# Performance work log

Measured on AMD Instinct MI355X. Metric: run time of the kernel, lower is better.

## Reference

```python
import jax, jax.numpy as jnp
import numpy as np

B, N, E, D_IN, D_OUT = 16, 2048, 65536, 256, 256


def setup_inputs() -> dict:
    key = jax.random.key(0)
    k1, k2, k3 = jax.random.split(key, 3)
    node_features = jax.random.normal(k1, (B, N, D_IN), dtype=jnp.float32)
    edge_indices = jax.random.randint(k2, (B, 2, E), 0, N, dtype=jnp.int64)
    W = jax.random.normal(k3, (D_OUT, 2 * D_IN), dtype=jnp.float32) * (1.0 / np.sqrt(2 * D_IN))
    b = jnp.zeros((D_OUT,), dtype=jnp.float32)
    return {"node_features": node_features, "edge_indices": edge_indices, "W": W, "b": b}


def reference(node_features, edge_indices, W, b):
    # node_features: [B, N, D]; edge_indices: [B, 2, E] (src row 0, dst row 1)
    n_nodes = node_features.shape[1]
    src = edge_indices[:, 0, :]  # [B, E]
    dst = edge_indices[:, 1, :]  # [B, E]
    # gather source-node features per edge: [B, E, D]
    gathered = jnp.take_along_axis(node_features, src[:, :, None], axis=1)

    def per_graph(feats_g, dst_g):
        s = jax.ops.segment_sum(feats_g, dst_g, num_segments=n_nodes)          # [N, D]
        c = jax.ops.segment_sum(jnp.ones_like(dst_g, dtype=feats_g.dtype),
                                dst_g, num_segments=n_nodes)                    # [N]
        return s / jnp.maximum(c, 1.0)[:, None]  # mean; 0 for isolated nodes

    neighbor_agg = jax.vmap(per_graph)(gathered, dst)            # [B, N, D]
    combined = jnp.concatenate([node_features, neighbor_agg], axis=-1)  # [B, N, 2D]
    return jnp.einsum('bnd,od->bno', combined, W) + b
```

## Files before the change

### kernel.cpp

```cpp
#include <hip/hip_runtime.h>
#include <hip/hip_bf16.h>

#define BATCH 16
#define NNODE 2048
#define NEDGE 65536
#define DIN   256
#define DOUT  256
#define KDIM  512
#define SUB   16
#define ESUB  (NEDGE/SUB)

typedef __attribute__((ext_vector_type(8))) short short8;
typedef __attribute__((ext_vector_type(8))) ushort ushort8;
typedef __attribute__((ext_vector_type(4))) float f32x4;

__device__ __forceinline__ ushort f2bf(float f) {
    union { float f; unsigned u; } v; v.f = f;
    unsigned u = v.u;
    unsigned r = (u + 0x7fffu + ((u >> 16) & 1u)) >> 16;
    return (ushort)r;
}

__device__ __forceinline__ int q8(float x) {
    float c = fminf(fmaxf(x * 16.0f, -127.0f), 127.0f);
    return (int)rintf(c);
}

#define ASYNC_COPY16(gsrc, ldst) \
    __builtin_amdgcn_global_load_lds((const __attribute__((address_space(1))) void*)(gsrc), \
                                     (__attribute__((address_space(3))) void*)(ldst), 16, 0, 0)

__global__ __launch_bounds__(256) void prep_kernel(
        const float* __restrict__ X, const float* __restrict__ W,
        const int* __restrict__ E,
        int* __restrict__ partial,
        ushort* __restrict__ Xbf, unsigned char* __restrict__ Xi8,
        ushort* __restrict__ Wbf) {
    int bid = blockIdx.x;
    int t = threadIdx.x;
    if (bid < 256) {
        __shared__ int hist[NNODE];
        int b = bid & 15, sub = bid >> 4;
#pragma unroll
        for (int j = 0; j < 8; ++j) hist[t + j * 256] = 0;
        __syncthreads();
        const int4* dsts = reinterpret_cast<const int4*>(
            E + (size_t)b * 2 * NEDGE + NEDGE + sub * ESUB);
#pragma unroll
        for (int j = 0; j < 4; ++j) {
            int4 d = dsts[j * 256 + t];
            atomicAdd(&hist[d.x], 1);
            atomicAdd(&hist[d.y], 1);
            atomicAdd(&hist[d.z], 1);
            atomicAdd(&hist[d.w], 1);
        }
        __syncthreads();
        int* pb = partial + ((size_t)b * SUB + sub) * NNODE;
#pragma unroll
        for (int j = 0; j < 8; ++j) pb[t + j * 256] = hist[t + j * 256];
    } else if (bid < 4352) {
        size_t i = (size_t)(bid - 256) * 256 + t;
        const float4* p = reinterpret_cast<const float4*>(X + i * 8);
        float4 u = p[0], v = p[1];
        ushort4 o0 = { f2bf(u.x), f2bf(u.y), f2bf(u.z), f2bf(u.w) };
        ushort4 o1 = { f2bf(v.x), f2bf(v.y), f2bf(v.z), f2bf(v.w) };
        *reinterpret_cast<ushort4*>(Xbf + i * 8)     = o0;
        *reinterpret_cast<ushort4*>(Xbf + i * 8 + 4) = o1;
        unsigned q0 = (q8(u.x) & 255) | ((q8(u.y) & 255) << 8) |
                      ((q8(u.z) & 255) << 16) | ((unsigned)(q8(u.w) & 255) << 24);
        unsigned q1 = (q8(v.x) & 255) | ((q8(v.y) & 255) << 8) |
                      ((q8(v.z) & 255) << 16) | ((unsigned)(q8(v.w) & 255) << 24);
        uint2 q = { q0, q1 };
        *reinterpret_cast<uint2*>(Xi8 + i * 8) = q;
    } else {
        size_t i = (size_t)(bid - 4352) * 256 + t;
        const float4* p = reinterpret_cast<const float4*>(W + i * 8);
        float4 u = p[0], v = p[1];
        ushort4 o0 = { f2bf(u.x), f2bf(u.y), f2bf(u.z), f2bf(u.w) };
        ushort4 o1 = { f2bf(v.x), f2bf(v.y), f2bf(v.z), f2bf(v.w) };
        *reinterpret_cast<ushort4*>(Wbf + i * 8)     = o0;
        *reinterpret_cast<ushort4*>(Wbf + i * 8 + 4) = o1;
    }
}

__global__ __launch_bounds__(256) void fillscan_kernel(
        const int* __restrict__ E,
        const int* __restrict__ partial,
        int* __restrict__ counts, int* __restrict__ cursor,
        int* __restrict__ srcIdx) {
    __shared__ int cur[NNODE];
    __shared__ int tsum[256];
    int bid = blockIdx.x;
    int t = threadIdx.x;
    int b = bid & 15, sub = bid >> 4;
    const int* pb = partial + (size_t)b * SUB * NNODE;

    int tot[8] = {}, pre[8] = {};
    for (int k = 0; k < SUB; ++k) {
        const int4* p = reinterpret_cast<const int4*>(pb + k * NNODE + t * 8);
        int4 a = p[0], c = p[1];
        if (k < sub) {
            pre[0] += a.x; pre[1] += a.y; pre[2] += a.z; pre[3] += a.w;
            pre[4] += c.x; pre[5] += c.y; pre[6] += c.z; pre[7] += c.w;
        }
        tot[0] += a.x; tot[1] += a.y; tot[2] += a.z; tot[3] += a.w;
        tot[4] += c.x; tot[5] += c.y; tot[6] += c.z; tot[7] += c.w;
    }
    int s = 0;
#pragma unroll
    for (int j = 0; j < 8; ++j) s += tot[j];
    tsum[t] = s;
    __syncthreads();
    for (int off = 1; off < 256; off <<= 1) {
        int v = (t >= off) ? tsum[t - off] : 0;
        __syncthreads();
        tsum[t] += v;
        __syncthreads();
    }
    int run = (t == 0) ? 0 : tsum[t - 1];
    bool writer = (sub == 0);
    int base = b * NNODE + t * 8;
#pragma unroll
    for (int j = 0; j < 8; ++j) {
        cur[t * 8 + j] = run + pre[j];
        if (writer) { counts[base + j] = tot[j]; cursor[base + j] = run; }
        run += tot[j];
    }
    __syncthreads();

    const int* eb = E + (size_t)b * 2 * NEDGE;
    const int4* srcs = reinterpret_cast<const int4*>(eb + sub * ESUB);
    const int4* dsts = reinterpret_cast<const int4*>(eb + NEDGE + sub * ESUB);
    int* sb = srcIdx + (size_t)b * NEDGE;
#pragma unroll
    for (int j = 0; j < 4; ++j) {
        int4 sv = srcs[j * 256 + t];
        int4 dv = dsts[j * 256 + t];
        sb[atomicAdd(&cur[dv.x], 1)] = sv.x;
        sb[atomicAdd(&cur[dv.y], 1)] = sv.y;
        sb[atomicAdd(&cur[dv.z], 1)] = sv.z;
        sb[atomicAdd(&cur[dv.w], 1)] = sv.w;
    }
}

__global__ __launch_bounds__(256) void aggregate_kernel(
        const unsigned char* __restrict__ Xi8,
        const int* __restrict__ srcIdx,
        const int* __restrict__ cursor,
        const int* __restrict__ counts,
        ushort* __restrict__ Gbf) {
    int bid = blockIdx.x;
    int blk = (bid & 7) * 1024 + (bid >> 3);
    int wave = threadIdx.x >> 6;
    int lane = threadIdx.x & 63;
    int q = lane >> 4;
    int l16 = lane & 15;
    int f0 = l16 * 16;
    int node = blk * 4 + wave;
    int b = node >> 11;
    int deg = counts[node];
    int start = cursor[node];
    const unsigned char* xb = Xi8 + (size_t)b * NNODE * DIN;
    const int* sidx = srcIdx + (size_t)b * NEDGE + start;

    unsigned a0 = 0, a1 = 0, a2 = 0, a3 = 0, a4 = 0, a5 = 0, a6 = 0, a7 = 0;
#define M16 0x00FF00FFu
#define ACC16(v) do {                                                         \
        unsigned w0 = (v).x ^ 0x80808080u, w1 = (v).y ^ 0x80808080u;          \
        unsigned w2 = (v).z ^ 0x80808080u, w3 = (v).w ^ 0x80808080u;          \
        a0 += w0 & M16;  a1 += (w0 >> 8) & M16;                               \
        a2 += w1 & M16;  a3 += (w1 >> 8) & M16;                               \
        a4 += w2 & M16;  a5 += (w2 >> 8) & M16;                               \
        a6 += w3 & M16;  a7 += (w3 >> 8) & M16;                               \
    } while (0)

    int i = 0;
    for (; i + 16 <= deg; i += 16) {
        int s0 = sidx[i + q], s1 = sidx[i + 4 + q];
        int s2 = sidx[i + 8 + q], s3 = sidx[i + 12 + q];
        uint4 v0 = *reinterpret_cast<const uint4*>(xb + (size_t)s0 * DIN + f0);
        uint4 v1 = *reinterpret_cast<const uint4*>(xb + (size_t)s1 * DIN + f0);
        uint4 v2 = *reinterpret_cast<const uint4*>(xb + (size_t)s2 * DIN + f0);
        uint4 v3 = *reinterpret_cast<const uint4*>(xb + (size_t)s3 * DIN + f0);
        ACC16(v0); ACC16(v1); ACC16(v2); ACC16(v3);
    }
    for (; i < deg; i += 4) {
        int e = i + q;
        uint4 v = { 0x80808080u, 0x80808080u, 0x80808080u, 0x80808080u };
        if (e < deg) {
            int s0 = sidx[e];
            v = *reinterpret_cast<const uint4*>(xb + (size_t)s0 * DIN + f0);
        }
        ACC16(v);
    }
#undef ACC16
    a0 += (unsigned)__shfl_xor((int)a0, 16, 64); a0 += (unsigned)__shfl_xor((int)a0, 32, 64);
    a1 += (unsigned)__shfl_xor((int)a1, 16, 64); a1 += (unsigned)__shfl_xor((int)a1, 32, 64);
    a2 += (unsigned)__shfl_xor((int)a2, 16, 64); a2 += (unsigned)__shfl_xor((int)a2, 32, 64);
    a3 += (unsigned)__shfl_xor((int)a3, 16, 64); a3 += (unsigned)__shfl_xor((int)a3, 32, 64);
    a4 += (unsigned)__shfl_xor((int)a4, 16, 64); a4 += (unsigned)__shfl_xor((int)a4, 32, 64);
    a5 += (unsigned)__shfl_xor((int)a5, 16, 64); a5 += (unsigned)__shfl_xor((int)a5, 32, 64);
    a6 += (unsigned)__shfl_xor((int)a6, 16, 64); a6 += (unsigned)__shfl_xor((int)a6, 32, 64);
    a7 += (unsigned)__shfl_xor((int)a7, 16, 64); a7 += (unsigned)__shfl_xor((int)a7, 32, 64);

    if (q == 0) {
        float sc = 1.0f / (16.0f * (float)max(deg, 1));
        float bias = 128.0f * (float)deg;
        float f[16];
        f[ 0] = ((float)(int)(a0 & 0xFFFFu) - bias) * sc;
        f[ 2] = ((float)(int)(a0 >> 16)     - bias) * sc;
        f[ 1] = ((float)(int)(a1 & 0xFFFFu) - bias) * sc;
        f[ 3] = ((float)(int)(a1 >> 16)     - bias) * sc;
        f[ 4] = ((float)(int)(a2 & 0xFFFFu) - bias) * sc;
        f[ 6] = ((float)(int)(a2 >> 16)     - bias) * sc;
        f[ 5] = ((float)(int)(a3 & 0xFFFFu) - bias) * sc;
        f[ 7] = ((float)(int)(a3 >> 16)     - bias) * sc;
        f[ 8] = ((float)(int)(a4 & 0xFFFFu) - bias) * sc;
        f[10] = ((float)(int)(a4 >> 16)     - bias) * sc;
        f[ 9] = ((float)(int)(a5 & 0xFFFFu) - bias) * sc;
        f[11] = ((float)(int)(a5 >> 16)     - bias) * sc;
        f[12] = ((float)(int)(a6 & 0xFFFFu) - bias) * sc;
        f[14] = ((float)(int)(a6 >> 16)     - bias) * sc;
        f[13] = ((float)(int)(a7 & 0xFFFFu) - bias) * sc;
        f[15] = ((float)(int)(a7 >> 16)     - bias) * sc;
        ushort8 o0, o1;
#pragma unroll
        for (int j = 0; j < 8; ++j) { o0[j] = f2bf(f[j]); o1[j] = f2bf(f[j + 8]); }
        ushort* gp = Gbf + (size_t)node * DIN + f0;
        *reinterpret_cast<ushort8*>(gp)     = o0;
        *reinterpret_cast<ushort8*>(gp + 8) = o1;
    }
}

__global__ __launch_bounds__(256) void gemm_kernel(
        const ushort* __restrict__ Xbf,
        const ushort* __restrict__ Gbf,
        const ushort* __restrict__ Wbf,
        const float* __restrict__ bias,
        float* __restrict__ out) {
    __shared__ ushort As[3][128 * 32];
    __shared__ ushort Bs[3][128 * 32];
    const int tid = threadIdx.x;
    const int wid = tid >> 6, lane = tid & 63;

    int orig = blockIdx.x;
    int logical = (orig & 7) * 64 + (orig >> 3);
    int bx = logical >> 1;
    int by = logical & 1;
    const int rowBase = bx * 128;
    const int colBase = by * 128;
    const int wm = wid >> 1, wn = wid & 1;

    f32x4 acc[4][4] = {};

    const int lr = lane >> 2;
    const int lk = (((lane & 3) ^ ((lane >> 3) & 3)) * 8);

    const ushort* Arow = Xbf + (size_t)rowBase * DIN;
    const ushort* Grow = Gbf + (size_t)rowBase * DIN;
    const ushort* Brow = Wbf + (size_t)colBase * KDIM;
    const int r0 = wid * 16 + lr;

#define STAGE(k0, buf) do {                                                   \
        const ushort* Ab = ((k0) < DIN) ? (Arow + (k0)) : (Grow + ((k0) - DIN)); \
        const ushort* Bb = Brow + (k0);                                       \
        ASYNC_COPY16(Ab + (size_t)r0 * DIN + lk,          &As[buf][wid * 512]);       \
        ASYNC_COPY16(Ab + (size_t)(r0 + 64) * DIN + lk,   &As[buf][2048 + wid * 512]);\
        ASYNC_COPY16(Bb + (size_t)r0 * KDIM + lk,         &Bs[buf][wid * 512]);       \
        ASYNC_COPY16(Bb + (size_t)(r0 + 64) * KDIM + lk,  &Bs[buf][2048 + wid * 512]);\
    } while (0)

    const int fl = lane & 15;
    const int fc = ((lane >> 4) ^ ((fl >> 1) & 3)) * 8;

    STAGE(0, 0);
    STAGE(32, 1);
    for (int t = 0; t < 16; ++t) {
        const int bt = t % 3;
        if (t + 2 < 16) {
            STAGE((t + 2) * 32, (t + 2) % 3);
            asm volatile("s_waitcnt vmcnt(8)" ::: "memory");
        } else if (t + 1 < 16) {
            asm volatile("s_waitcnt vmcnt(4)" ::: "memory");
        } else {
            asm volatile("s_waitcnt vmcnt(0)" ::: "memory");
        }
        __builtin_amdgcn_s_barrier();

        short8 a[4], b[4];
#pragma unroll
        for (int m = 0; m < 4; ++m)
            a[m] = *reinterpret_cast<const short8*>(
                &As[bt][(wm * 64 + m * 16 + fl) * 32 + fc]);
#pragma unroll
        for (int n = 0; n < 4; ++n)
            b[n] = *reinterpret_cast<const short8*>(
                &Bs[bt][(wn * 64 + n * 16 + fl) * 32 + fc]);
#pragma unroll
        for (int m = 0; m < 4; ++m)
#pragma unroll
            for (int n = 0; n < 4; ++n)
                acc[m][n] = __builtin_amdgcn_mfma_f32_16x16x32_bf16(
                    a[m], b[n], acc[m][n], 0, 0, 0);
        __builtin_amdgcn_s_barrier();
    }
#undef STAGE

    const int cl = lane & 15, rq = lane >> 4;
#pragma unroll
    for (int n = 0; n < 4; ++n) {
        int col = colBase + wn * 64 + n * 16 + cl;
        float bv = bias[col];
#pragma unroll
        for (int m = 0; m < 4; ++m) {
            int r0o = rowBase + wm * 64 + m * 16 + rq * 4;
#pragma unroll
            for (int j = 0; j < 4; ++j)
                out[(size_t)(r0o + j) * DOUT + col] = acc[m][n][j] + bv;
        }
    }
}

extern "C" void kernel_launch(void* const* d_in, const int* in_sizes, int n_in,
                              void* d_out, int out_size, void* d_ws, size_t ws_size,
                              hipStream_t stream) {
    const float* X    = (const float*)d_in[0];
    const int*   E    = (const int*)d_in[1];
    const float* W    = (const float*)d_in[2];
    const float* bias = (const float*)d_in[3];
    float* out = (float*)d_out;

    char* ws = (char*)d_ws;
    ushort* Xbf  = (ushort*)ws;
    ushort* Gbf  = Xbf + (size_t)BATCH * NNODE * DIN;
    ushort* Wbf  = Gbf + (size_t)BATCH * NNODE * DIN;
    int* counts  = (int*)(Wbf + (size_t)DOUT * KDIM);
    int* cursor  = counts + BATCH * NNODE;
    int* srcIdx  = cursor + BATCH * NNODE;
    unsigned char* Xi8 = (unsigned char*)(srcIdx + (size_t)BATCH * NEDGE);
    int* partial = (int*)Gbf;

    prep_kernel<<<4416, 256, 0, stream>>>(X, W, E, partial, Xbf, Xi8, Wbf);

    fillscan_kernel<<<256, 256, 0, stream>>>(E, partial, counts, cursor, srcIdx);

    aggregate_kernel<<<(BATCH * NNODE) / 4, 256, 0, stream>>>(
        Xi8, srcIdx, cursor, counts, Gbf);

    dim3 ggrid(512);
    gemm_kernel<<<ggrid, 256, 0, stream>>>(Xbf, Gbf, Wbf, bias, out);
}
```

Before: 66.91 us.

## Fuse neighbor aggregation into GEMM with FP8 aggregated half in LDS

Removes the separate aggregate kernel and the bf16 G buffer round trip through global memory. Each 512-thread GEMM block now computes the mean-aggregated neighbor features for its 128 rows, quantizes them to FP8 e4m3 in LDS, and runs the second half of K with fp8 MFMA against an FP8 pre-swizzled copy of W. Blocks cover all 256 output columns, so each gathers its rows once. In exchange the gather latency is no longer overlapped with other blocks' GEMM, there are only 256 blocks, and FP8 costs accuracy.

```diff
diff --git a/kernel.cpp b/kernel.cpp
--- a/kernel.cpp
+++ b/kernel.cpp
@@ -11,7 +11,6 @@
 #define ESUB  (NEDGE/SUB)
 
 typedef __attribute__((ext_vector_type(8))) short short8;
-typedef __attribute__((ext_vector_type(8))) ushort ushort8;
 typedef __attribute__((ext_vector_type(4))) float f32x4;
 
 __device__ __forceinline__ ushort f2bf(float f) {
@@ -26,6 +25,36 @@
     return (int)rintf(c);
 }
 
+__device__ __forceinline__ unsigned f2e4m3(float x) {
+    unsigned u = __float_as_uint(x);
+    unsigned s = (u >> 24) & 0x80u;
+    float ax = __uint_as_float(u & 0x7FFFFFFFu);
+    if (ax >= 448.0f) return s | 0x7Eu;
+    if (ax < 0.0009765625f) return s;
+    if (ax < 0.015625f) {
+        int q = (int)rintf(ax * 512.0f);
+        return s | (unsigned)q;
+    }
+    unsigned au = __float_as_uint(ax);
+    int e = (int)((au >> 23) & 0xFF) - 127;
+    unsigned m = au & 0x7FFFFFu;
+    unsigned keep = m >> 20;
+    unsigned rest = m & 0xFFFFFu;
+    keep += (rest > 0x80000u) || (rest == 0x80000u && (keep & 1u));
+    unsigned val = ((unsigned)(e + 7) << 3) + keep;
+    if (val > 0x7Eu) val = 0x7Eu;
+    return s | val;
+}
+template <bool HI>
+__device__ __forceinline__ unsigned pk2_fp8(float a, float b, unsigned old) {
+#if __has_builtin(__builtin_amdgcn_cvt_pk_fp8_f32)
+    return (unsigned)__builtin_amdgcn_cvt_pk_fp8_f32(a, b, (int)old, HI);
+#else
+    unsigned p = f2e4m3(a) | (f2e4m3(b) << 8);
+    return HI ? ((old & 0xFFFFu) | (p << 16)) : ((old & 0xFFFF0000u) | p);
+#endif
+}
+
 #define ASYNC_COPY16(gsrc, ldst) \
     __builtin_amdgcn_global_load_lds((const __attribute__((address_space(1))) void*)(gsrc), \
                                      (__attribute__((address_space(3))) void*)(ldst), 16, 0, 0)
@@ -35,7 +64,7 @@
         const int* __restrict__ E,
         int* __restrict__ partial,
         ushort* __restrict__ Xbf, unsigned char* __restrict__ Xi8,
-        ushort* __restrict__ Wbf) {
+        ushort* __restrict__ Wbf, unsigned char* __restrict__ Wf8s) {
     int bid = blockIdx.x;
     int t = threadIdx.x;
     if (bid < 256) {
@@ -73,13 +102,26 @@
         uint2 q = { q0, q1 };
         *reinterpret_cast<uint2*>(Xi8 + i * 8) = q;
     } else {
-        size_t i = (size_t)(bid - 4352) * 256 + t;
-        const float4* p = reinterpret_cast<const float4*>(W + i * 8);
+        int i = (bid - 4352) * 256 + t;
+        int col = i >> 6;
+        int k = (i & 63) * 8;
+        const float4* p = reinterpret_cast<const float4*>(W + (size_t)col * KDIM + k);
         float4 u = p[0], v = p[1];
-        ushort4 o0 = { f2bf(u.x), f2bf(u.y), f2bf(u.z), f2bf(u.w) };
-        ushort4 o1 = { f2bf(v.x), f2bf(v.y), f2bf(v.z), f2bf(v.w) };
-        *reinterpret_cast<ushort4*>(Wbf + i * 8)     = o0;
-        *reinterpret_cast<ushort4*>(Wbf + i * 8 + 4) = o1;
+        if (k < DIN) {
+            ushort4 o0 = { f2bf(u.x), f2bf(u.y), f2bf(u.z), f2bf(u.w) };
+            ushort4 o1 = { f2bf(v.x), f2bf(v.y), f2bf(v.z), f2bf(v.w) };
+            *reinterpret_cast<ushort4*>(Wbf + (size_t)col * KDIM + k)     = o0;
+            *reinterpret_cast<ushort4*>(Wbf + (size_t)col * KDIM + k + 4) = o1;
+        } else {
+            unsigned w0 = pk2_fp8<false>(u.x, u.y, 0u);
+            w0 = pk2_fp8<true>(u.z, u.w, w0);
+            unsigned w1 = pk2_fp8<false>(v.x, v.y, 0u);
+            w1 = pk2_fp8<true>(v.z, v.w, w1);
+            int kk = k - DIN;
+            int kt = kk >> 5, kq = (kk >> 3) & 3;
+            uint2 qv = { w0, w1 };
+            *reinterpret_cast<uint2*>(Wf8s + (size_t)kt * 8192 + kq * 2048 + col * 8) = qv;
+        }
     }
 }
 
@@ -143,27 +185,50 @@
     }
 }
 
-__global__ __launch_bounds__(256) void aggregate_kernel(
+__global__ __launch_bounds__(512, 4) void gemm_fused(
+        const ushort* __restrict__ Xbf,
         const unsigned char* __restrict__ Xi8,
+        const ushort* __restrict__ Wbf,
+        const unsigned char* __restrict__ Wf8s,
         const int* __restrict__ srcIdx,
         const int* __restrict__ cursor,
         const int* __restrict__ counts,
-        ushort* __restrict__ Gbf) {
-    int bid = blockIdx.x;
-    int blk = (bid & 7) * 1024 + (bid >> 3);
-    int wave = threadIdx.x >> 6;
-    int lane = threadIdx.x & 63;
-    int q = lane >> 4;
-    int l16 = lane & 15;
-    int f0 = l16 * 16;
-    int node = blk * 4 + wave;
-    int b = node >> 11;
-    int deg = counts[node];
-    int start = cursor[node];
-    const unsigned char* xb = Xi8 + (size_t)b * NNODE * DIN;
-    const int* sidx = srcIdx + (size_t)b * NEDGE + start;
-
-    unsigned a0 = 0, a1 = 0, a2 = 0, a3 = 0, a4 = 0, a5 = 0, a6 = 0, a7 = 0;
+        const float* __restrict__ bias,
+        float* __restrict__ out) {
+    __shared__ ushort As[2][128 * 32];
+    __shared__ ushort Bs[2][256 * 32];
+    __shared__ uint4  GqV[2048];
+
+    const int tid = threadIdx.x;
+    const int wid = tid >> 6, lane = tid & 63;
+    const int wm = wid >> 2, wn = wid & 3;
+
+    int orig = blockIdx.x;
+    int logical = (orig & 7) * 32 + (orig >> 3);
+    const int rowBase = logical * 128;
+    const int b = rowBase >> 11;
+
+    f32x4 acc[4][4] = {};
+
+    const int r0 = wid * 16 + (lane >> 2);
+    const int lk = (((lane & 3) ^ ((lane >> 3) & 3)) * 8);
+    const ushort* Arow = Xbf + (size_t)rowBase * DIN;
+
+#define STAGE_X(k0, buf) do {                                                  \
+        ASYNC_COPY16(Arow + (size_t)r0 * DIN + (k0) + lk,         &As[buf][wid * 512]);        \
+        ASYNC_COPY16(Wbf + (size_t)r0 * KDIM + (k0) + lk,         &Bs[buf][wid * 512]);        \
+        ASYNC_COPY16(Wbf + (size_t)(r0 + 128) * KDIM + (k0) + lk, &Bs[buf][4096 + wid * 512]); \
+    } while (0)
+#define STAGE_G(kt, fbuf) \
+        ASYNC_COPY16(Wf8s + (size_t)(kt) * 8192 + (size_t)(wid * 64 + lane) * 16, \
+                     &Bs[fbuf][wid * 512])
+
+    STAGE_X(0, 0);
+
+    {
+        const int q = lane >> 4, l16 = lane & 15;
+        const int f0 = l16 * 16;
+        const unsigned char* xb = Xi8 + (size_t)b * NNODE * DIN;
 #define M16 0x00FF00FFu
 #define ACC16(v) do {                                                         \
         unsigned w0 = (v).x ^ 0x80808080u, w1 = (v).y ^ 0x80808080u;          \
@@ -173,143 +238,141 @@
         a4 += w2 & M16;  a5 += (w2 >> 8) & M16;                               \
         a6 += w3 & M16;  a7 += (w3 >> 8) & M16;                               \
     } while (0)
-
-    int i = 0;
-    for (; i + 16 <= deg; i += 16) {
-        int s0 = sidx[i + q], s1 = sidx[i + 4 + q];
-        int s2 = sidx[i + 8 + q], s3 = sidx[i + 12 + q];
-        uint4 v0 = *reinterpret_cast<const uint4*>(xb + (size_t)s0 * DIN + f0);
-        uint4 v1 = *reinterpret_cast<const uint4*>(xb + (size_t)s1 * DIN + f0);
-        uint4 v2 = *reinterpret_cast<const uint4*>(xb + (size_t)s2 * DIN + f0);
-        uint4 v3 = *reinterpret_cast<const uint4*>(xb + (size_t)s3 * DIN + f0);
-        ACC16(v0); ACC16(v1); ACC16(v2); ACC16(v3);
-    }
-    for (; i < deg; i += 4) {
-        int e = i + q;
-        uint4 v = { 0x80808080u, 0x80808080u, 0x80808080u, 0x80808080u };
-        if (e < deg) {
-            int s0 = sidx[e];
-            v = *reinterpret_cast<const uint4*>(xb + (size_t)s0 * DIN + f0);
-        }
-        ACC16(v);
-    }
+        for (int nn = 0; nn < 16; ++nn) {
+            int r = wid * 16 + nn;
+            int node = rowBase + r;
+            int deg = counts[node];
+            int start = cursor[node];
+            const int* sidx = srcIdx + (size_t)b * NEDGE + start;
+            unsigned a0 = 0, a1 = 0, a2 = 0, a3 = 0, a4 = 0, a5 = 0, a6 = 0, a7 = 0;
+            int i = 0;
+            for (; i + 16 <= deg; i += 16) {
+                int s0 = sidx[i + q], s1 = sidx[i + 4 + q];
+                int s2 = sidx[i + 8 + q], s3 = sidx[i + 12 + q];
+                uint4 v0 = *reinterpret_cast<const uint4*>(xb + (size_t)s0 * DIN + f0);
+                uint4 v1 = *reinterpret_cast<const uint4*>(xb + (size_t)s1 * DIN + f0);
+                uint4 v2 = *reinterpret_cast<const uint4*>(xb + (size_t)s2 * DIN + f0);
+                uint4 v3 = *reinterpret_cast<const uint4*>(xb + (size_t)s3 * DIN + f0);
+                ACC16(v0); ACC16(v1); ACC16(v2); ACC16(v3);
+            }
+            for (; i < deg; i += 4) {
+                int e = i + q;
+                uint4 v = { 0x80808080u, 0x80808080u, 0x80808080u, 0x80808080u };
+                if (e < deg)
+                    v = *reinterpret_cast<const uint4*>(xb + (size_t)sidx[e] * DIN + f0);
+                ACC16(v);
+            }
+            a0 += (unsigned)__shfl_xor((int)a0, 16, 64); a0 += (unsigned)__shfl_xor((int)a0, 32, 64);
+            a1 += (unsigned)__shfl_xor((int)a1, 16, 64); a1 += (unsigned)__shfl_xor((int)a1, 32, 64);
+            a2 += (unsigned)__shfl_xor((int)a2, 16, 64); a2 += (unsigned)__shfl_xor((int)a2, 32, 64);
+            a3 += (unsigned)__shfl_xor((int)a3, 16, 64); a3 += (unsigned)__shfl_xor((int)a3, 32, 64);
+            a4 += (unsigned)__shfl_xor((int)a4, 16, 64); a4 += (unsigned)__shfl_xor((int)a4, 32, 64);
+            a5 += (unsigned)__shfl_xor((int)a5, 16, 64); a5 += (unsigned)__shfl_xor((int)a5, 32, 64);
+            a6 += (unsigned)__shfl_xor((int)a6, 16, 64); a6 += (unsigned)__shfl_xor((int)a6, 32, 64);
+            a7 += (unsigned)__shfl_xor((int)a7, 16, 64); a7 += (unsigned)__shfl_xor((int)a7, 32, 64);
+            if (q == 0) {
+                float sc = 1.0f / (16.0f * (float)max(deg, 1));
+                float bs = 128.0f * (float)deg;
+                float f[16];
+                f[ 0] = ((float)(int)(a0 & 0xFFFFu) - bs) * sc;
+                f[ 2] = ((float)(int)(a0 >> 16)     - bs) * sc;
+                f[ 1] = ((float)(int)(a1 & 0xFFFFu) - bs) * sc;
+                f[ 3] = ((float)(int)(a1 >> 16)     - bs) * sc;
+                f[ 4] = ((float)(int)(a2 & 0xFFFFu) - bs) * sc;
+                f[ 6] = ((float)(int)(a2 >> 16)     - bs) * sc;
+                f[ 5] = ((float)(int)(a3 & 0xFFFFu) - bs) * sc;
+                f[ 7] = ((float)(int)(a3 >> 16)     - bs) * sc;
+                f[ 8] = ((float)(int)(a4 & 0xFFFFu) - bs) * sc;
+                f[10] = ((float)(int)(a4 >> 16)     - bs) * sc;
+                f[ 9] = ((float)(int)(a5 & 0xFFFFu) - bs) * sc;
+                f[11] = ((float)(int)(a5 >> 16)     - bs) * sc;
+                f[12] = ((float)(int)(a6 & 0xFFFFu) - bs) * sc;
+                f[14] = ((float)(int)(a6 >> 16)     - bs) * sc;
+                f[13] = ((float)(int)(a7 & 0xFFFFu) - bs) * sc;
+                f[15] = ((float)(int)(a7 >> 16)     - bs) * sc;
+                unsigned wds[4];
+#pragma unroll
+                for (int w = 0; w < 4; ++w) {
+                    unsigned t0 = pk2_fp8<false>(f[4 * w], f[4 * w + 1], 0u);
+                    wds[w] = pk2_fp8<true>(f[4 * w + 2], f[4 * w + 3], t0);
+                }
+                int slot = l16 ^ ((r >> 1) & 7);
+                uint4 val;
+                if (r & 1) { val.x = wds[2]; val.y = wds[3]; val.z = wds[0]; val.w = wds[1]; }
+                else       { val.x = wds[0]; val.y = wds[1]; val.z = wds[2]; val.w = wds[3]; }
+                GqV[r * 16 + slot] = val;
+            }
+        }
 #undef ACC16
-    a0 += (unsigned)__shfl_xor((int)a0, 16, 64); a0 += (unsigned)__shfl_xor((int)a0, 32, 64);
-    a1 += (unsigned)__shfl_xor((int)a1, 16, 64); a1 += (unsigned)__shfl_xor((int)a1, 32, 64);
-    a2 += (unsigned)__shfl_xor((int)a2, 16, 64); a2 += (unsigned)__shfl_xor((int)a2, 32, 64);
-    a3 += (unsigned)__shfl_xor((int)a3, 16, 64); a3 += (unsigned)__shfl_xor((int)a3, 32, 64);
-    a4 += (unsigned)__shfl_xor((int)a4, 16, 64); a4 += (unsigned)__shfl_xor((int)a4, 32, 64);
-    a5 += (unsigned)__shfl_xor((int)a5, 16, 64); a5 += (unsigned)__shfl_xor((int)a5, 32, 64);
-    a6 += (unsigned)__shfl_xor((int)a6, 16, 64); a6 += (unsigned)__shfl_xor((int)a6, 32, 64);
-    a7 += (unsigned)__shfl_xor((int)a7, 16, 64); a7 += (unsigned)__shfl_xor((int)a7, 32, 64);
-
-    if (q == 0) {
-        float sc = 1.0f / (16.0f * (float)max(deg, 1));
-        float bias = 128.0f * (float)deg;
-        float f[16];
-        f[ 0] = ((float)(int)(a0 & 0xFFFFu) - bias) * sc;
-        f[ 2] = ((float)(int)(a0 >> 16)     - bias) * sc;
-        f[ 1] = ((float)(int)(a1 & 0xFFFFu) - bias) * sc;
-        f[ 3] = ((float)(int)(a1 >> 16)     - bias) * sc;
-        f[ 4] = ((float)(int)(a2 & 0xFFFFu) - bias) * sc;
-        f[ 6] = ((float)(int)(a2 >> 16)     - bias) * sc;
-        f[ 5] = ((float)(int)(a3 & 0xFFFFu) - bias) * sc;
-        f[ 7] = ((float)(int)(a3 >> 16)     - bias) * sc;
-        f[ 8] = ((float)(int)(a4 & 0xFFFFu) - bias) * sc;
-        f[10] = ((float)(int)(a4 >> 16)     - bias) * sc;
-        f[ 9] = ((float)(int)(a5 & 0xFFFFu) - bias) * sc;
-        f[11] = ((float)(int)(a5 >> 16)     - bias) * sc;
-        f[12] = ((float)(int)(a6 & 0xFFFFu) - bias) * sc;
-        f[14] = ((float)(int)(a6 >> 16)     - bias) * sc;
-        f[13] = ((float)(int)(a7 & 0xFFFFu) - bias) * sc;
-        f[15] = ((float)(int)(a7 >> 16)     - bias) * sc;
-        ushort8 o0, o1;
-#pragma unroll
-        for (int j = 0; j < 8; ++j) { o0[j] = f2bf(f[j]); o1[j] = f2bf(f[j + 8]); }
-        ushort* gp = Gbf + (size_t)node * DIN + f0;
-        *reinterpret_cast<ushort8*>(gp)     = o0;
-        *reinterpret_cast<ushort8*>(gp + 8) = o1;
-    }
-}
-
-__global__ __launch_bounds__(256) void gemm_kernel(
-        const ushort* __restrict__ Xbf,
-        const ushort* __restrict__ Gbf,
-        const ushort* __restrict__ Wbf,
-        const float* __restrict__ bias,
-        float* __restrict__ out) {
-    __shared__ ushort As[3][128 * 32];
-    __shared__ ushort Bs[3][128 * 32];
-    const int tid = threadIdx.x;
-    const int wid = tid >> 6, lane = tid & 63;
-
-    int orig = blockIdx.x;
-    int logical = (orig & 7) * 64 + (orig >> 3);
-    int bx = logical >> 1;
-    int by = logical & 1;
-    const int rowBase = bx * 128;
-    const int colBase = by * 128;
-    const int wm = wid >> 1, wn = wid & 1;
-
-    f32x4 acc[4][4] = {};
-
-    const int lr = lane >> 2;
-    const int lk = (((lane & 3) ^ ((lane >> 3) & 3)) * 8);
-
-    const ushort* Arow = Xbf + (size_t)rowBase * DIN;
-    const ushort* Grow = Gbf + (size_t)rowBase * DIN;
-    const ushort* Brow = Wbf + (size_t)colBase * KDIM;
-    const int r0 = wid * 16 + lr;
-
-#define STAGE(k0, buf) do {                                                   \
-        const ushort* Ab = ((k0) < DIN) ? (Arow + (k0)) : (Grow + ((k0) - DIN)); \
-        const ushort* Bb = Brow + (k0);                                       \
-        ASYNC_COPY16(Ab + (size_t)r0 * DIN + lk,          &As[buf][wid * 512]);       \
-        ASYNC_COPY16(Ab + (size_t)(r0 + 64) * DIN + lk,   &As[buf][2048 + wid * 512]);\
-        ASYNC_COPY16(Bb + (size_t)r0 * KDIM + lk,         &Bs[buf][wid * 512]);       \
-        ASYNC_COPY16(Bb + (size_t)(r0 + 64) * KDIM + lk,  &Bs[buf][2048 + wid * 512]);\
-    } while (0)
+#undef M16
+    }
+    __syncthreads();
 
     const int fl = lane & 15;
-    const int fc = ((lane >> 4) ^ ((fl >> 1) & 3)) * 8;
-
-    STAGE(0, 0);
-    STAGE(32, 1);
+    const int kq = lane >> 4;
+    const int fc = (kq ^ ((fl >> 1) & 3)) * 8;
+    const long* GqL = reinterpret_cast<const long*>(GqV);
+
     for (int t = 0; t < 16; ++t) {
-        const int bt = t % 3;
-        if (t + 2 < 16) {
-            STAGE((t + 2) * 32, (t + 2) % 3);
-            asm volatile("s_waitcnt vmcnt(8)" ::: "memory");
-        } else if (t + 1 < 16) {
-            asm volatile("s_waitcnt vmcnt(4)" ::: "memory");
+        if (t < 7) {
+            STAGE_X((t + 1) * 32, (t + 1) & 1);
+            asm volatile("s_waitcnt vmcnt(3)" ::: "memory");
+        } else if (t < 15) {
+            STAGE_G(t - 7, (t - 7) & 1);
+            asm volatile("s_waitcnt vmcnt(1)" ::: "memory");
         } else {
             asm volatile("s_waitcnt vmcnt(0)" ::: "memory");
         }
         __builtin_amdgcn_s_barrier();
 
-        short8 a[4], b[4];
-#pragma unroll
-        for (int m = 0; m < 4; ++m)
-            a[m] = *reinterpret_cast<const short8*>(
-                &As[bt][(wm * 64 + m * 16 + fl) * 32 + fc]);
-#pragma unroll
-        for (int n = 0; n < 4; ++n)
-            b[n] = *reinterpret_cast<const short8*>(
-                &Bs[bt][(wn * 64 + n * 16 + fl) * 32 + fc]);
-#pragma unroll
-        for (int m = 0; m < 4; ++m)
+        if (t < 8) {
+            const int bufx = t & 1;
+            short8 a[4], bb[4];
+#pragma unroll
+            for (int m = 0; m < 4; ++m)
+                a[m] = *reinterpret_cast<const short8*>(
+                    &As[bufx][(wm * 64 + m * 16 + fl) * 32 + fc]);
 #pragma unroll
             for (int n = 0; n < 4; ++n)
-                acc[m][n] = __builtin_amdgcn_mfma_f32_16x16x32_bf16(
-                    a[m], b[n], acc[m][n], 0, 0, 0);
+                bb[n] = *reinterpret_cast<const short8*>(
+                    &Bs[bufx][(wn * 64 + n * 16 + fl) * 32 + fc]);
+#pragma unroll
+            for (int m = 0; m < 4; ++m)
+#pragma unroll
+                for (int n = 0; n < 4; ++n)
+                    acc[m][n] = __builtin_amdgcn_mfma_f32_16x16x32_bf16(
+                        a[m], bb[n], acc[m][n], 0, 0, 0);
+        } else {
+            const int kt = t - 8;
+            const unsigned char* Bf8 =
+                reinterpret_cast<const unsigned char*>(&Bs[kt & 1][0]);
+            long ag[4], bg[4];
+#pragma unroll
+            for (int m = 0; m < 4; ++m) {
+                int r = wm * 64 + m * 16 + fl;
+                ag[m] = GqL[r * 32 + ((kt * 4 + kq) ^ (r & 15))];
+            }
+#pragma unroll
+            for (int n = 0; n < 4; ++n) {
+                int c = wn * 64 + n * 16 + fl;
+                bg[n] = *reinterpret_cast<const long*>(Bf8 + kq * 2048 + c * 8);
+            }
+#pragma unroll
+            for (int m = 0; m < 4; ++m)
+#pragma unroll
+                for (int n = 0; n < 4; ++n)
+                    acc[m][n] = __builtin_amdgcn_mfma_f32_16x16x32_fp8_fp8(
+                        ag[m], bg[n], acc[m][n], 0, 0, 0);
+        }
         __builtin_amdgcn_s_barrier();
     }
-#undef STAGE
+#undef STAGE_X
+#undef STAGE_G
 
     const int cl = lane & 15, rq = lane >> 4;
 #pragma unroll
     for (int n = 0; n < 4; ++n) {
-        int col = colBase + wn * 64 + n * 16 + cl;
+        int col = wn * 64 + n * 16 + cl;
         float bv = bias[col];
 #pragma unroll
         for (int m = 0; m < 4; ++m) {
@@ -332,21 +395,18 @@
 
     char* ws = (char*)d_ws;
     ushort* Xbf  = (ushort*)ws;
-    ushort* Gbf  = Xbf + (size_t)BATCH * NNODE * DIN;
-    ushort* Wbf  = Gbf + (size_t)BATCH * NNODE * DIN;
-    int* counts  = (int*)(Wbf + (size_t)DOUT * KDIM);
+    unsigned char* Xi8 = (unsigned char*)(Xbf + (size_t)BATCH * NNODE * DIN);
+    ushort* Wbf  = (ushort*)(Xi8 + (size_t)BATCH * NNODE * DIN);
+    unsigned char* Wf8s = (unsigned char*)(Wbf + (size_t)DOUT * KDIM);
+    int* counts  = (int*)(Wf8s + 8 * 8192);
     int* cursor  = counts + BATCH * NNODE;
     int* srcIdx  = cursor + BATCH * NNODE;
-    unsigned char* Xi8 = (unsigned char*)(srcIdx + (size_t)BATCH * NEDGE);
-    int* partial = (int*)Gbf;
-
-    prep_kernel<<<4416, 256, 0, stream>>>(X, W, E, partial, Xbf, Xi8, Wbf);
+    int* partial = srcIdx + (size_t)BATCH * NEDGE;
+
+    prep_kernel<<<4416, 256, 0, stream>>>(X, W, E, partial, Xbf, Xi8, Wbf, Wf8s);
 
     fillscan_kernel<<<256, 256, 0, stream>>>(E, partial, counts, cursor, srcIdx);
 
-    aggregate_kernel<<<(BATCH * NNODE) / 4, 256, 0, stream>>>(
-        Xi8, srcIdx, cursor, counts, Gbf);
-
-    dim3 ggrid(512);
-    gemm_kernel<<<ggrid, 256, 0, stream>>>(Xbf, Gbf, Wbf, bias, out);
-}
+    gemm_fused<<<256, 512, 0, stream>>>(Xbf, Xi8, Wbf, Wf8s,
+                                        srcIdx, cursor, counts, bias, out);
+}
```

Measured after the change: 81.53 us. +21.8%, slower.
